# Optimization experiments

Measured on AMD Instinct MI355X. Metric: run time of the kernel, lower is better.

## Reference

```python
import jax, jax.numpy as jnp
import numpy as np

N_NODES = 50000
N_EDGES = 800000
D = 128


def _dense_params(key, d_in, d_out):
    kw, kb = jax.random.split(key)
    W = jax.random.normal(kw, (d_in, d_out), dtype=jnp.float32) / np.sqrt(d_in)
    b = jnp.zeros((d_out,), dtype=jnp.float32)
    return W, b


def setup_inputs() -> dict:
    key = jax.random.key(0)
    ks = jax.random.split(key, 9)
    nodes = jax.random.normal(ks[0], (N_NODES, D), dtype=jnp.float32)
    edges = jax.random.normal(ks[1], (N_EDGES, D), dtype=jnp.float32)
    senders = jax.random.randint(ks[2], (N_EDGES,), 0, N_NODES, dtype=jnp.int32)
    receivers = jax.random.randint(ks[3], (N_EDGES,), 0, N_NODES, dtype=jnp.int32)
    W_s1, b_s1 = _dense_params(ks[4], D, D)   # Dense on nodes -> sent_attributes_1
    W_r, b_r = _dense_params(ks[5], D, D)     # Dense on nodes -> received_attributes
    W_e, b_e = _dense_params(ks[6], D, D)     # Dense on edges
    W_att, b_att = _dense_params(ks[7], D, 1) # attention Dense -> scalar per edge
    W_m, b_m = _dense_params(ks[8], D, D)     # Dense on message (simple_update)
    return {
        "nodes": nodes, "edges": edges, "senders": senders, "receivers": receivers,
        "W_s1": W_s1, "b_s1": b_s1, "W_r": W_r, "b_r": b_r,
        "W_e": W_e, "b_e": b_e, "W_att": W_att, "b_att": b_att,
        "W_m": W_m, "b_m": b_m,
    }


def reference(nodes, edges, senders, receivers,
              W_s1, b_s1, W_r, b_r, W_e, b_e, W_att, b_att, W_m, b_m):
    n = nodes.shape[0]
    # dense projections on nodes, then gather along edges
    sent_1 = (nodes @ W_s1 + b_s1)[senders]          # [E, D]
    received = (nodes @ W_r + b_r)[receivers]        # [E, D]
    sent_2 = nodes[senders]                          # [E, D] (simple_update: raw gather)
    e_proj = edges @ W_e + b_e                       # [E, D]
    edges_new = sent_1 + e_proj + received           # add_features=True
    # attention: Dense(1) + leaky_relu, segment softmax over receivers
    att = jax.nn.leaky_relu(edges_new @ W_att + b_att)          # [E, 1]
    seg_max = jax.ops.segment_max(att, receivers, num_segments=n)
    expv = jnp.exp(att - seg_max[receivers])
    denom = jax.ops.segment_sum(expv, receivers, num_segments=n)
    weights = expv / denom[receivers]                            # [E, 1]
    # message: Dense on gathered sender features, weighted scatter-sum
    message = weights * (sent_2 @ W_m + b_m)                     # [E, D]
    nodes_new = jax.ops.segment_sum(message, receivers, num_segments=n)  # [N, D]
    return nodes_new, edges_new
```

## Files before the change

kernel.cpp:

```cpp
#include <hip/hip_runtime.h>
#include <hip/hip_bf16.h>
#include <cstdint>
#include <cstddef>

#define NN 50000
#define NE 800000
#define DD 128

typedef __attribute__((ext_vector_type(8))) short short8;
typedef __attribute__((ext_vector_type(4))) float f32x4;

__device__ __forceinline__ unsigned short f2bf(float f) {
  unsigned u = __float_as_uint(f);
  u = (u + 0x7FFFu + ((u >> 16) & 1u)) >> 16;
  return (unsigned short)u;
}

__global__ void k_prep(const float* __restrict__ Ws1, const float* __restrict__ Wr,
                       const float* __restrict__ Wm, const float* __restrict__ We,
                       unsigned short* __restrict__ Wt) {
  int i = blockIdx.x * blockDim.x + threadIdx.x;
  for (int idx = i; idx < 4 * DD * DD; idx += gridDim.x * blockDim.x) {
    int m = idx >> 14, r = idx & 16383, col = r >> 7, k = r & 127;
    const float* src = (m == 0) ? Ws1 : (m == 1) ? Wr : (m == 2) ? Wm : We;
    Wt[idx] = f2bf(src[k * DD + col]);
  }
}

__device__ __forceinline__ unsigned cvtpk(float lo, float hi) {
  unsigned r;
  asm("v_cvt_pk_bf16_f32 %0, %1, %2" : "=v"(r) : "v"(lo), "v"(hi));
  return r;
}

__device__ __forceinline__ short8 cvt8(f32x4 f0, f32x4 f1) {
  union { short8 s; unsigned u[4]; } t;
  t.u[0] = cvtpk(f0[0], f0[1]);
  t.u[1] = cvtpk(f0[2], f0[3]);
  t.u[2] = cvtpk(f1[0], f1[1]);
  t.u[3] = cvtpk(f1[2], f1[3]);
  return t.s;
}

__device__ __forceinline__ f32x4 unpk(uint2 u) {
  f32x4 v;
  v[0] = __uint_as_float(u.x << 16);
  v[1] = __uint_as_float(u.x & 0xFFFF0000u);
  v[2] = __uint_as_float(u.y << 16);
  v[3] = __uint_as_float(u.y & 0xFFFF0000u);
  return v;
}

__device__ __forceinline__ void stage_w(const unsigned short* __restrict__ Wt,
                                        char* __restrict__ lds, int tid) {
#pragma unroll
  for (int c = 0; c < 8; ++c) {
    int ci = tid * 8 + c;
    int col = ci >> 4, slot = ci & 15;
    uint4 v = *(const uint4*)(Wt + ci * 8);
    *(uint4*)(lds + col * 256 + ((slot ^ col) & 15) * 16) = v;
  }
}

__device__ __forceinline__ short8 read_w(const char* __restrict__ lds, int col, int slot) {
  return *(const short8*)(lds + col * 256 + ((slot ^ col) & 15) * 16);
}

__global__ __launch_bounds__(256, 4) void k_nodeproj(
    const float* __restrict__ nodes, const unsigned short* __restrict__ Wt,
    const float* __restrict__ b_s1, const float* __restrict__ b_r, const float* __restrict__ b_m,
    const float* __restrict__ b_e,
    unsigned* __restrict__ P1h, unsigned* __restrict__ Prh, unsigned* __restrict__ Pmh) {
  __shared__ char ldsW[32768];
  int m = blockIdx.y;
  int tid = threadIdx.x;
  stage_w(Wt + m * 16384, ldsW, tid);
  __syncthreads();
  const float* bias = (m == 0) ? b_s1 : (m == 1) ? b_r : b_m;
  unsigned* P = (m == 0) ? P1h : (m == 1) ? Prh : Pmh;
  int wid = tid >> 6, l = tid & 63;
  int lmod = l & 15, ldiv = l >> 4;
  int wave = blockIdx.x * 4 + wid, nw = gridDim.x * 4;
  for (int b = wave; b < NN / 16; b += nw) {
    int row = b * 16 + lmod;
    const float* nrow = nodes + (size_t)row * DD;
    short8 bb[4];
#pragma unroll
    for (int kk = 0; kk < 4; ++kk) {
      const f32x4* p = (const f32x4*)(nrow + kk * 32 + ldiv * 8);
      bb[kk] = cvt8(p[0], p[1]);
    }
    f32x4 acc[8] = {};
#pragma unroll
    for (int kk = 0; kk < 4; ++kk) {
#pragma unroll
      for (int rb = 0; rb < 8; ++rb) {
        short8 a = read_w(ldsW, rb * 16 + lmod, kk * 4 + ldiv);
        acc[rb] = __builtin_amdgcn_mfma_f32_16x16x32_bf16(a, bb[kk], acc[rb], 0, 0, 0);
      }
    }
#pragma unroll
    for (int rb = 0; rb < 8; ++rb) {
      int d0 = rb * 16 + ldiv * 4;
      f32x4 bv = *(const f32x4*)(bias + d0);
      if (m == 0) {
        f32x4 be = *(const f32x4*)(b_e + d0);
#pragma unroll
        for (int j = 0; j < 4; ++j) bv[j] += be[j];
      }
      f32x4 v = acc[rb];
#pragma unroll
      for (int j = 0; j < 4; ++j) v[j] += bv[j];
      uint2 pk;
      pk.x = cvtpk(v[0], v[1]);
      pk.y = cvtpk(v[2], v[3]);
      *(uint2*)(P + (size_t)row * (DD / 2) + d0 / 2) = pk;
    }
  }
}

__global__ __launch_bounds__(256, 3) void k_edge(
    const float* __restrict__ edges, const int* __restrict__ senders,
    const int* __restrict__ receivers, const unsigned short* __restrict__ WtE,
    const unsigned* __restrict__ P1h, const unsigned* __restrict__ Prh,
    const float* __restrict__ W_att, const float* __restrict__ b_att,
    float* __restrict__ out_edges, float* __restrict__ attb, int* __restrict__ cnt) {
  __shared__ char ldsW[32768];
  __shared__ float attw[DD];
  int tid = threadIdx.x;
  stage_w(WtE, ldsW, tid);
  if (tid < DD / 4) ((f32x4*)attw)[tid] = ((const f32x4*)W_att)[tid];
  __syncthreads();
  int wid = tid >> 6, l = tid & 63;
  int lmod = l & 15, ldiv = l >> 4;
  int wave = blockIdx.x * 4 + wid, nw = gridDim.x * 4;
  const int NB = NE / 16;
  float batt = b_att[0];

  int b = wave;
  if (b >= NB) return;

  f32x4 A[8], B[8];
  int sA, rcA, sB, rcB;

  auto load_grp = [&](f32x4(&G)[8], int& S, int& R, int bt) {
    int en = bt * 16 + lmod;
    const f32x4* erow = (const f32x4*)(edges + (size_t)en * DD);
#pragma unroll
    for (int q = 0; q < 8; ++q)
      G[q] = __builtin_nontemporal_load(erow + ((q >> 1) * 8 + ldiv * 2 + (q & 1)));
    S = senders[en];
    R = receivers[en];
  };

  auto body = [&](f32x4(&CUR)[8], int& SC, int& RC, f32x4(&NXT)[8], int& SN, int& RN) {
    int e = b * 16 + lmod;
    const unsigned* p1 = P1h + (size_t)SC * (DD / 2);
    const unsigned* pr = Prh + (size_t)RC * (DD / 2);
    uint2 g1[8], gr[8];
#pragma unroll
    for (int rb = 0; rb < 8; ++rb) {
      int d2 = rb * 8 + ldiv * 2;
      g1[rb] = *(const uint2*)(p1 + d2);
      gr[rb] = *(const uint2*)(pr + d2);
    }
    int bn = b + nw;
    if (bn < NB) load_grp(NXT, SN, RN, bn);
    short8 bb[4];
#pragma unroll
    for (int kk = 0; kk < 4; ++kk) bb[kk] = cvt8(CUR[2 * kk], CUR[2 * kk + 1]);
    f32x4 acc[8] = {};
#pragma unroll
    for (int kk = 0; kk < 4; ++kk) {
#pragma unroll
      for (int rb = 0; rb < 8; ++rb) {
        short8 a = read_w(ldsW, rb * 16 + lmod, kk * 4 + ldiv);
        acc[rb] = __builtin_amdgcn_mfma_f32_16x16x32_bf16(a, bb[kk], acc[rb], 0, 0, 0);
      }
    }
    float* oe = out_edges + (size_t)e * DD;
    float att = 0.f;
#pragma unroll
    for (int rb = 0; rb < 8; ++rb) {
      int d0 = rb * 16 + ldiv * 4;
      f32x4 g1v = unpk(g1[rb]);
      f32x4 grv = unpk(gr[rb]);
      f32x4 wa = *(const f32x4*)(attw + d0);
      f32x4 v = acc[rb];
#pragma unroll
      for (int j = 0; j < 4; ++j) {
        float x = v[j] + g1v[j] + grv[j];
        v[j] = x;
        att += x * wa[j];
      }
      __builtin_nontemporal_store(v, (f32x4*)(oe + d0));
    }
    att += __shfl_xor(att, 16);
    att += __shfl_xor(att, 32);
    if (ldiv == 0) {
      float av = att + batt;
      av = (av >= 0.f) ? av : 0.01f * av;
      attb[e] = av;
      atomicAdd(&cnt[RC], 1);
    }
    b = bn;
  };

  load_grp(A, sA, rcA, b);
  while (true) {
    body(A, sA, rcA, B, sB, rcB);
    if (b >= NB) break;
    body(B, sB, rcB, A, sA, rcA);
    if (b >= NB) break;
  }
}

__global__ __launch_bounds__(1024) void k_scan(const int* __restrict__ cnt,
                                               int* __restrict__ offs) {
  __shared__ int wsum[16];
  __shared__ int sbase;
  int t = threadIdx.x;
  int lane = t & 63, wid = t >> 6;
  if (t == 0) { sbase = 0; offs[0] = 0; }
  __syncthreads();
  for (int c = 0; c < 13; ++c) {
    int i0 = c * 4096 + t * 4;
    int v0 = 0, v1 = 0, v2 = 0, v3 = 0;
    if (i0 + 3 < NN) {
      int4 v = *(const int4*)(cnt + i0);
      v0 = v.x; v1 = v.y; v2 = v.z; v3 = v.w;
    } else {
      if (i0 + 0 < NN) v0 = cnt[i0 + 0];
      if (i0 + 1 < NN) v1 = cnt[i0 + 1];
      if (i0 + 2 < NN) v2 = cnt[i0 + 2];
      if (i0 + 3 < NN) v3 = cnt[i0 + 3];
    }
    int p1 = v0, p2 = p1 + v1, p3 = p2 + v2, p4 = p3 + v3;
    int x = p4;
#pragma unroll
    for (int d = 1; d < 64; d <<= 1) {
      int o = __shfl_up(x, d, 64);
      if (lane >= d) x += o;
    }
    if (lane == 63) wsum[wid] = x;
    int excl_lane = x - p4;
    __syncthreads();
    int wbase = 0, tot = 0;
#pragma unroll
    for (int w2 = 0; w2 < 16; ++w2) {
      int sv = wsum[w2];
      if (w2 < wid) wbase += sv;
      tot += sv;
    }
    int base = sbase + wbase + excl_lane;
    if (i0 + 0 < NN) offs[i0 + 1] = base + p1;
    if (i0 + 1 < NN) offs[i0 + 2] = base + p2;
    if (i0 + 2 < NN) offs[i0 + 3] = base + p3;
    if (i0 + 3 < NN) offs[i0 + 4] = base + p4;
    __syncthreads();
    if (t == 0) sbase += tot;
    __syncthreads();
  }
}

__global__ void k_fill(const int* __restrict__ receivers, const int* __restrict__ offs,
                       int* __restrict__ cursor, int* __restrict__ eidx) {
  int e = blockIdx.x * 256 + threadIdx.x;
  if (e < NE) {
    int rc = receivers[e];
    int pos = offs[rc] + atomicAdd(&cursor[rc], 1);
    eidx[pos] = e;
  }
}

__global__ __launch_bounds__(256) void k_node(
    const int* __restrict__ offs, const int* __restrict__ eidx,
    const int* __restrict__ senders, const float* __restrict__ attb,
    const unsigned* __restrict__ Pmh, float* __restrict__ out_nodes) {
  int wid = threadIdx.x >> 6, l = threadIdx.x & 63;
  int n = blockIdx.x * 4 + wid;
  if (n >= NN) return;
  int start = offs[n], end = offs[n + 1];
  float m = -3.4e38f, denom = 0.f, ax = 0.f, ay = 0.f;
  for (int c = start; c < end; c += 64) {
    int rem = end - c;
    if (rem > 64) rem = 64;
    float a_l = -3.4e38f;
    int s_l = 0;
    if (l < rem) {
      int e = eidx[c + l];
      a_l = attb[e];
      s_l = senders[e];
    }
    float cm = a_l;
#pragma unroll
    for (int d = 1; d < 64; d <<= 1) cm = fmaxf(cm, __shfl_xor(cm, d));
    if (cm > m) {
      float sc = __expf(m - cm);
      denom *= sc; ax *= sc; ay *= sc;
      m = cm;
    }
#pragma unroll 8
    for (int i = 0; i < rem; ++i) {
      float a = __shfl(a_l, i);
      int s = __shfl(s_l, i);
      float w = __expf(a - m);
      denom += w;
      unsigned u = Pmh[(size_t)s * (DD / 2) + l];
      float vx = __uint_as_float(u << 16);
      float vy = __uint_as_float(u & 0xFFFF0000u);
      ax += w * vx;
      ay += w * vy;
    }
  }
  float2 o = {0.f, 0.f};
  if (end > start) {
    float inv = 1.f / denom;
    o.x = ax * inv;
    o.y = ay * inv;
  }
  *(float2*)(out_nodes + (size_t)n * DD + l * 2) = o;
}

extern "C" void kernel_launch(void* const* d_in, const int* in_sizes, int n_in,
                              void* d_out, int out_size, void* d_ws, size_t ws_size,
                              hipStream_t stream) {
  (void)in_sizes; (void)n_in; (void)out_size; (void)ws_size;
  const float* nodes = (const float*)d_in[0];
  const float* edges = (const float*)d_in[1];
  const int* senders = (const int*)d_in[2];
  const int* receivers = (const int*)d_in[3];
  const float* W_s1 = (const float*)d_in[4];
  const float* b_s1 = (const float*)d_in[5];
  const float* W_r = (const float*)d_in[6];
  const float* b_r = (const float*)d_in[7];
  const float* W_e = (const float*)d_in[8];
  const float* b_e = (const float*)d_in[9];
  const float* W_att = (const float*)d_in[10];
  const float* b_att = (const float*)d_in[11];
  const float* W_m = (const float*)d_in[12];
  const float* b_m = (const float*)d_in[13];

  float* out_nodes = (float*)d_out;
  float* out_edges = out_nodes + (size_t)NN * DD;

  char* w = (char*)d_ws;
  unsigned short* Wt = (unsigned short*)w; w += (size_t)4 * DD * DD * 2;
  unsigned* P1h = (unsigned*)w; w += (size_t)NN * (DD / 2) * 4;
  unsigned* Prh = (unsigned*)w; w += (size_t)NN * (DD / 2) * 4;
  unsigned* Pmh = (unsigned*)w; w += (size_t)NN * (DD / 2) * 4;
  float* attb = (float*)w; w += (size_t)NE * 4;
  int* eidx = (int*)w; w += (size_t)NE * 4;
  int* cnt = (int*)w; w += (size_t)NN * 4;
  int* cursor = (int*)w; w += (size_t)NN * 4;
  int* offs = (int*)w; w += (size_t)(NN + 1) * 4;

  hipMemsetAsync(cnt, 0, (size_t)NN * 8, stream);

  k_prep<<<64, 256, 0, stream>>>(W_s1, W_r, W_m, W_e, Wt);
  k_nodeproj<<<dim3(256, 3), 256, 0, stream>>>(nodes, Wt, b_s1, b_r, b_m, b_e, P1h, Prh, Pmh);
  k_edge<<<768, 256, 0, stream>>>(edges, senders, receivers, Wt + 3 * 16384,
                                  P1h, Prh, W_att, b_att, out_edges, attb, cnt);
  k_scan<<<1, 1024, 0, stream>>>(cnt, offs);
  k_fill<<<(NE + 255) / 256, 256, 0, stream>>>(receivers, offs, cursor, eidx);
  k_node<<<NN / 4, 256, 0, stream>>>(offs, eidx, senders, attb, Pmh, out_nodes);
}
```

Measured before the change: 452.3 us.

## Single-buffer edge prefetch and process four edges per wave in node aggregation

The edge kernel drops the A/B double-buffered register sets and uses one register buffer. It issues the next group's loads right after converting the current group to bf16, which lowers register pressure and may raise occupancy. The node kernel now splits each wave into four 16-lane groups that each handle a different edge with 16-byte row loads, then reduces across groups. The softmax denominator is computed once per chunk with a wave reduction instead of per edge. This gives more memory parallelism per wave in the gather but adds cross-lane shuffles at the end.

```diff
diff --git a/kernel.cpp b/kernel.cpp
--- a/kernel.cpp
+++ b/kernel.cpp
@@ -140,23 +140,23 @@
   int b = wave;
   if (b >= NB) return;
 
-  f32x4 A[8], B[8];
-  int sA, rcA, sB, rcB;
-
-  auto load_grp = [&](f32x4(&G)[8], int& S, int& R, int bt) {
-    int en = bt * 16 + lmod;
+  f32x4 E[8];
+  int s, rc;
+  {
+    int en = b * 16 + lmod;
     const f32x4* erow = (const f32x4*)(edges + (size_t)en * DD);
 #pragma unroll
     for (int q = 0; q < 8; ++q)
-      G[q] = __builtin_nontemporal_load(erow + ((q >> 1) * 8 + ldiv * 2 + (q & 1)));
-    S = senders[en];
-    R = receivers[en];
-  };
-
-  auto body = [&](f32x4(&CUR)[8], int& SC, int& RC, f32x4(&NXT)[8], int& SN, int& RN) {
+      E[q] = __builtin_nontemporal_load(erow + ((q >> 1) * 8 + ldiv * 2 + (q & 1)));
+    s = senders[en];
+    rc = receivers[en];
+  }
+
+  while (b < NB) {
     int e = b * 16 + lmod;
-    const unsigned* p1 = P1h + (size_t)SC * (DD / 2);
-    const unsigned* pr = Prh + (size_t)RC * (DD / 2);
+    int bn = b + nw;
+    const unsigned* p1 = P1h + (size_t)s * (DD / 2);
+    const unsigned* pr = Prh + (size_t)rc * (DD / 2);
     uint2 g1[8], gr[8];
 #pragma unroll
     for (int rb = 0; rb < 8; ++rb) {
@@ -164,11 +164,19 @@
       g1[rb] = *(const uint2*)(p1 + d2);
       gr[rb] = *(const uint2*)(pr + d2);
     }
-    int bn = b + nw;
-    if (bn < NB) load_grp(NXT, SN, RN, bn);
+    int rc0 = rc;
     short8 bb[4];
 #pragma unroll
-    for (int kk = 0; kk < 4; ++kk) bb[kk] = cvt8(CUR[2 * kk], CUR[2 * kk + 1]);
+    for (int kk = 0; kk < 4; ++kk) bb[kk] = cvt8(E[2 * kk], E[2 * kk + 1]);
+    if (bn < NB) {
+      int en = bn * 16 + lmod;
+      const f32x4* erow = (const f32x4*)(edges + (size_t)en * DD);
+#pragma unroll
+      for (int q = 0; q < 8; ++q)
+        E[q] = __builtin_nontemporal_load(erow + ((q >> 1) * 8 + ldiv * 2 + (q & 1)));
+      s = senders[en];
+      rc = receivers[en];
+    }
     f32x4 acc[8] = {};
 #pragma unroll
     for (int kk = 0; kk < 4; ++kk) {
@@ -201,17 +209,9 @@
       float av = att + batt;
       av = (av >= 0.f) ? av : 0.01f * av;
       attb[e] = av;
-      atomicAdd(&cnt[RC], 1);
+      atomicAdd(&cnt[rc0], 1);
     }
     b = bn;
-  };
-
-  load_grp(A, sA, rcA, b);
-  while (true) {
-    body(A, sA, rcA, B, sB, rcB);
-    if (b >= NB) break;
-    body(B, sB, rcB, A, sA, rcA);
-    if (b >= NB) break;
   }
 }
 
@@ -281,7 +281,9 @@
   int n = blockIdx.x * 4 + wid;
   if (n >= NN) return;
   int start = offs[n], end = offs[n + 1];
-  float m = -3.4e38f, denom = 0.f, ax = 0.f, ay = 0.f;
+  int g = l >> 4, q = l & 15;
+  float m = -3.4e38f, denom = 0.f;
+  f32x4 sA = {0.f, 0.f, 0.f, 0.f}, sB = {0.f, 0.f, 0.f, 0.f};
   for (int c = start; c < end; c += 64) {
     int rem = end - c;
     if (rem > 64) rem = 64;
@@ -297,29 +299,48 @@
     for (int d = 1; d < 64; d <<= 1) cm = fmaxf(cm, __shfl_xor(cm, d));
     if (cm > m) {
       float sc = __expf(m - cm);
-      denom *= sc; ax *= sc; ay *= sc;
+      denom *= sc;
+#pragma unroll
+      for (int j = 0; j < 4; ++j) { sA[j] *= sc; sB[j] *= sc; }
       m = cm;
     }
-#pragma unroll 8
-    for (int i = 0; i < rem; ++i) {
-      float a = __shfl(a_l, i);
-      int s = __shfl(s_l, i);
-      float w = __expf(a - m);
-      denom += w;
-      unsigned u = Pmh[(size_t)s * (DD / 2) + l];
-      float vx = __uint_as_float(u << 16);
-      float vy = __uint_as_float(u & 0xFFFF0000u);
-      ax += w * vx;
-      ay += w * vy;
-    }
-  }
-  float2 o = {0.f, 0.f};
-  if (end > start) {
-    float inv = 1.f / denom;
-    o.x = ax * inv;
-    o.y = ay * inv;
-  }
-  *(float2*)(out_nodes + (size_t)n * DD + l * 2) = o;
+    float ex = (l < rem) ? __expf(a_l - m) : 0.f;
+#pragma unroll
+    for (int d = 1; d < 64; d <<= 1) ex += __shfl_xor(ex, d);
+    denom += ex;
+    for (int i = 0; i < rem; i += 4) {
+      int ig = i + g;
+      float a = __shfl(a_l, ig & 63);
+      int sv = __shfl(s_l, ig & 63);
+      if (ig < rem) {
+        float w = __expf(a - m);
+        uint4 u = *(const uint4*)(Pmh + (size_t)sv * (DD / 2) + q * 4);
+        sA[0] += w * __uint_as_float(u.x << 16);
+        sA[1] += w * __uint_as_float(u.x & 0xFFFF0000u);
+        sA[2] += w * __uint_as_float(u.y << 16);
+        sA[3] += w * __uint_as_float(u.y & 0xFFFF0000u);
+        sB[0] += w * __uint_as_float(u.z << 16);
+        sB[1] += w * __uint_as_float(u.z & 0xFFFF0000u);
+        sB[2] += w * __uint_as_float(u.w << 16);
+        sB[3] += w * __uint_as_float(u.w & 0xFFFF0000u);
+      }
+    }
+  }
+#pragma unroll
+  for (int j = 0; j < 4; ++j) {
+    sA[j] += __shfl_xor(sA[j], 16);
+    sA[j] += __shfl_xor(sA[j], 32);
+    sB[j] += __shfl_xor(sB[j], 16);
+    sB[j] += __shfl_xor(sB[j], 32);
+  }
+  if (g == 0) {
+    float inv = (end > start) ? 1.f / denom : 0.f;
+#pragma unroll
+    for (int j = 0; j < 4; ++j) { sA[j] *= inv; sB[j] *= inv; }
+    float* orow = out_nodes + (size_t)n * DD + q * 8;
+    *(f32x4*)(orow) = sA;
+    *(f32x4*)(orow + 4) = sB;
+  }
 }
 
 extern "C" void kernel_launch(void* const* d_in, const int* in_sizes, int n_in,
```

New measurement: 391.0 us. 1.16x faster.
